# Performance work log

Measured on AMD Instinct MI355X. Metric: run time of the kernel, lower is better.

The kernel has to match this reference:

```python
import jax, jax.numpy as jnp
import numpy as np

F = 256

def setup_inputs() -> dict:
    key = jax.random.key(0)
    ks = jax.random.split(key, 6)
    s = 1.0 / np.sqrt(F)
    x = jax.random.normal(ks[0], (16, 1024, F), dtype=jnp.float32)
    W_alpha = jax.random.uniform(ks[1], (F, F), minval=-s, maxval=s, dtype=jnp.float32)
    W_beta = jax.random.uniform(ks[2], (F, F), minval=-s, maxval=s, dtype=jnp.float32)
    W_unary = jax.random.uniform(ks[3], (F, F), minval=-s, maxval=s, dtype=jnp.float32)
    b_unary = jax.random.uniform(ks[4], (F,), minval=-s, maxval=s, dtype=jnp.float32)
    W_r = jax.random.uniform(ks[5], (F, F), minval=-s, maxval=s, dtype=jnp.float32)
    return {"x": x, "W_alpha": W_alpha, "W_beta": W_beta, "W_unary": W_unary, "b_unary": b_unary, "W_r": W_r}

def reference(x, W_alpha, W_beta, W_unary, b_unary, W_r):
    # x: [B, N, F]; torch Linear computes x @ W^T (+ b)
    B, N, _ = x.shape
    alpha = jnp.einsum('bnf,gf->bng', x, W_alpha)
    beta = jnp.einsum('bnf,gf->bng', x, W_beta)
    unary = jnp.einsum('bnf,gf->bng', x, W_unary) + b_unary
    # scores: alpha_i . beta_j, diagonal excluded (i == j skipped in loop)
    scores = jnp.einsum('bif,bjf->bij', alpha, beta)
    scores = scores * (1.0 - jnp.eye(N, dtype=x.dtype))
    att = jnp.einsum('bij,bjf->bif', scores, unary) / N
    out = jnp.einsum('bif,gf->big', att, W_r) + x
    return out
```

## Files before the change

### kernel.cpp

```cpp
#include <hip/hip_runtime.h>


typedef __bf16 bf16;
typedef float floatx4 __attribute__((ext_vector_type(4)));
typedef bf16 bf16x8 __attribute__((ext_vector_type(8)));
typedef bf16 bf16x4 __attribute__((ext_vector_type(4)));

constexpr int FD = 256;
constexpr int NB = 16;
constexpr int NN = 1024;
constexpr int RR = NB * NN;

__device__ __forceinline__ bf16x8 cvt8(float4 a, float4 b) {
    bf16x8 o = { (bf16)a.x, (bf16)a.y, (bf16)a.z, (bf16)a.w,
                 (bf16)b.x, (bf16)b.y, (bf16)b.z, (bf16)b.w };
    return o;
}

__global__ __launch_bounds__(256)
void prep(const float* __restrict__ Wu, const float* __restrict__ bu, const float* __restrict__ Wr,
          bf16* __restrict__ Wcb, float* __restrict__ bc)
{
    const int blk = blockIdx.x, tid = threadIdx.x;
    if (blk < 256) {
        const int j = blk;
        float acc = 0.0f;
        for (int g = 0; g < FD; g += 4) {
            float4 wr = *(const float4*)&Wr[j * FD + g];
            acc += wr.x * Wu[g * FD + tid] + wr.y * Wu[(g + 1) * FD + tid]
                 + wr.z * Wu[(g + 2) * FD + tid] + wr.w * Wu[(g + 3) * FD + tid];
        }
        Wcb[j * FD + tid] = (bf16)acc;
    } else {
        float s = 0.0f;
        for (int g = 0; g < FD; g++) s += Wr[tid * FD + g] * bu[g];
        bc[tid] = s;
    }
}

__global__ __launch_bounds__(256)
void proj3(const float* __restrict__ x,
           const float* __restrict__ Wa, const float* __restrict__ Wb, const bf16* __restrict__ Wc,
           bf16* __restrict__ alpha, bf16* __restrict__ U2,
           bf16* __restrict__ betaT, bf16* __restrict__ U2T,
           const float* __restrict__ bc, float* __restrict__ dpart)
{
    constexpr int BM = 128, BN = 64, BK = 32, LDK = 36;
    __shared__ bf16 As[BM][LDK];
    __shared__ bf16 Bs[3][BN][LDK];
    __shared__ bf16 Tr[8960];
    const int tid = threadIdx.x;
    const int wave = tid >> 6, lane = tid & 63;
    const int q = lane >> 4, l16 = lane & 15;
    const int bm = blockIdx.y * BM, bn = blockIdx.x * BN;

    const int rowA0 = tid >> 2,          k8A0 = (tid & 3) * 8;
    const int rowA1 = (tid + 256) >> 2,  k8A1 = (tid & 3) * 8;
    const int rowW  = tid >> 2,          k8W  = (tid & 3) * 8;

    bf16x8 pxa0, pxa1, pwa, pwb; int4 pwc;
#define PROJ_LOAD(KK) do { \
        const float* s0 = &x[(size_t)(bm + rowA0) * FD + (KK) + k8A0]; \
        pxa0 = cvt8(*(const float4*)s0, *(const float4*)(s0 + 4)); \
        const float* s1 = &x[(size_t)(bm + rowA1) * FD + (KK) + k8A1]; \
        pxa1 = cvt8(*(const float4*)s1, *(const float4*)(s1 + 4)); \
        const float* sa = &Wa[(size_t)(bn + rowW) * FD + (KK) + k8W]; \
        pwa = cvt8(*(const float4*)sa, *(const float4*)(sa + 4)); \
        const float* sb = &Wb[(size_t)(bn + rowW) * FD + (KK) + k8W]; \
        pwb = cvt8(*(const float4*)sb, *(const float4*)(sb + 4)); \
        pwc = *(const int4*)&Wc[(size_t)(bn + rowW) * FD + (KK) + k8W]; \
    } while (0)

    floatx4 acc[3][2][4] = {};
    PROJ_LOAD(0);

    for (int k0 = 0; k0 < FD; k0 += BK) {
        *(bf16x8*)&As[rowA0][k8A0] = pxa0;
        *(bf16x8*)&As[rowA1][k8A1] = pxa1;
        *(bf16x8*)&Bs[0][rowW][k8W] = pwa;
        *(bf16x8*)&Bs[1][rowW][k8W] = pwb;
        *(int4*)&Bs[2][rowW][k8W] = pwc;
        __syncthreads();
        if (k0 + BK < FD) PROJ_LOAD(k0 + BK);
        bf16x8 af[2];
        #pragma unroll
        for (int mi = 0; mi < 2; mi++)
            af[mi] = *(const bf16x8*)&As[wave * 32 + mi * 16 + l16][q * 8];
        #pragma unroll
        for (int w = 0; w < 3; w++) {
            bf16x8 bq[4];
            #pragma unroll
            for (int nj = 0; nj < 4; nj++)
                bq[nj] = *(const bf16x8*)&Bs[w][nj * 16 + l16][q * 8];
            #pragma unroll
            for (int mi = 0; mi < 2; mi++)
                #pragma unroll
                for (int nj = 0; nj < 4; nj++)
                    acc[w][mi][nj] = __builtin_amdgcn_mfma_f32_16x16x32_bf16(af[mi], bq[nj], acc[w][mi][nj], 0, 0, 0);
        }
        __syncthreads();
    }
#undef PROJ_LOAD

    const int b = bm >> 10, n0 = bm & (NN - 1);
    float bcv[4];
    #pragma unroll
    for (int nj = 0; nj < 4; nj++) bcv[nj] = bc[bn + nj * 16 + l16];

    #pragma unroll
    for (int mi = 0; mi < 2; mi++)
        #pragma unroll
        for (int i = 0; i < 4; i++) {
            float p = 0.0f;
            #pragma unroll
            for (int nj = 0; nj < 4; nj++)
                p += acc[0][mi][nj][i] * acc[1][mi][nj][i];
            #pragma unroll
            for (int off = 1; off < 16; off <<= 1) p += __shfl_xor(p, off);
            if (l16 == 0) {
                int m = bm + wave * 32 + mi * 16 + q * 4 + i;
                dpart[(size_t)blockIdx.x * RR + m] = p;
            }
        }

    #pragma unroll
    for (int pass = 0; pass < 2; pass++) {
        const int w = pass ? 2 : 0;
        __syncthreads();
        #pragma unroll
        for (int mi = 0; mi < 2; mi++)
            #pragma unroll
            for (int i = 0; i < 4; i++) {
                int ml = wave * 32 + mi * 16 + q * 4 + i;
                #pragma unroll
                for (int nj = 0; nj < 4; nj++) {
                    float v = acc[w][mi][nj][i];
                    if (w == 2) v += bcv[nj];
                    Tr[ml * 68 + nj * 16 + l16] = (bf16)v;
                }
            }
        __syncthreads();
        bf16* dst = pass ? U2 : alpha;
        #pragma unroll
        for (int it = 0; it < 4; it++) {
            int c = tid + it * 256;
            int row = c >> 3, chunk = c & 7;
            bf16x8 v = *(const bf16x8*)&Tr[row * 68 + chunk * 8];
            *(bf16x8*)&dst[(size_t)(bm + row) * FD + bn + chunk * 8] = v;
        }
    }

    #pragma unroll
    for (int pass = 0; pass < 2; pass++) {
        const int w = pass ? 2 : 1;
        __syncthreads();
        #pragma unroll
        for (int mi = 0; mi < 2; mi++)
            #pragma unroll
            for (int nj = 0; nj < 4; nj++) {
                bf16x4 v4;
                #pragma unroll
                for (int i = 0; i < 4; i++) {
                    float v = acc[w][mi][nj][i];
                    if (w == 2) v += bcv[nj];
                    v4[i] = (bf16)v;
                }
                *(bf16x4*)&Tr[(nj * 16 + l16) * 140 + wave * 32 + mi * 16 + q * 4] = v4;
            }
        __syncthreads();
        bf16* dst = (pass ? U2T : betaT) + (size_t)b * FD * NN;
        #pragma unroll
        for (int it = 0; it < 4; it++) {
            int c = tid + it * 256;
            int row = c >> 4, chunk = c & 15;
            bf16x8 v = *(const bf16x8*)&Tr[row * 140 + chunk * 8];
            *(bf16x8*)&dst[(size_t)(bn + row) * NN + n0 + chunk * 8] = v;
        }
    }
}

__global__ __launch_bounds__(256)
void m2_mfma(const bf16* __restrict__ U2T, const bf16* __restrict__ betaT, bf16* __restrict__ M2t)
{
    constexpr int LDK = 36;
    __shared__ bf16 As[64][LDK];
    __shared__ bf16 Bs[64][LDK];
    __shared__ bf16 Tr[64 * 68];
    const int tid = threadIdx.x;
    const int wave = tid >> 6, lane = tid & 63;
    const int q = lane >> 4, l16 = lane & 15;
    const int wj = wave >> 1, wk = wave & 1;
    const int b = blockIdx.z;
    const int bj = blockIdx.y * 64, bk = blockIdx.x * 64;
    const int row = tid >> 2, k8 = (tid & 3) * 8;
    const bf16* Arow = U2T + (size_t)b * FD * NN + (size_t)(bj + row) * NN + k8;
    const bf16* Brow = betaT + (size_t)b * FD * NN + (size_t)(bk + row) * NN + k8;

    int4 ra = *(const int4*)&Arow[0];
    int4 rb = *(const int4*)&Brow[0];
    floatx4 acc[2][2] = {};
    for (int n0 = 0; n0 < NN; n0 += 32) {
        *(int4*)&As[row][k8] = ra;
        *(int4*)&Bs[row][k8] = rb;
        __syncthreads();
        if (n0 + 32 < NN) { ra = *(const int4*)&Arow[n0 + 32]; rb = *(const int4*)&Brow[n0 + 32]; }
        bf16x8 af[2], bq[2];
        #pragma unroll
        for (int mi = 0; mi < 2; mi++)
            af[mi] = *(const bf16x8*)&As[wj * 32 + mi * 16 + l16][q * 8];
        #pragma unroll
        for (int kj = 0; kj < 2; kj++)
            bq[kj] = *(const bf16x8*)&Bs[wk * 32 + kj * 16 + l16][q * 8];
        #pragma unroll
        for (int mi = 0; mi < 2; mi++)
            #pragma unroll
            for (int kj = 0; kj < 2; kj++)
                acc[mi][kj] = __builtin_amdgcn_mfma_f32_16x16x32_bf16(af[mi], bq[kj], acc[mi][kj], 0, 0, 0);
        __syncthreads();
    }
    __syncthreads();
    #pragma unroll
    for (int mi = 0; mi < 2; mi++)
        #pragma unroll
        for (int i = 0; i < 4; i++) {
            int jl = wj * 32 + mi * 16 + q * 4 + i;
            #pragma unroll
            for (int kj = 0; kj < 2; kj++)
                Tr[jl * 68 + wk * 32 + kj * 16 + l16] = (bf16)acc[mi][kj][i];
        }
    __syncthreads();
    bf16* Mb = M2t + (size_t)b * FD * FD;
    #pragma unroll
    for (int it = 0; it < 2; it++) {
        int c = tid + it * 256;
        int r = c >> 3, chunk = c & 7;
        bf16x8 v = *(const bf16x8*)&Tr[r * 68 + chunk * 8];
        *(bf16x8*)&Mb[(size_t)(bj + r) * FD + bk + chunk * 8] = v;
    }
}

__global__ __launch_bounds__(256)
void final_mfma(const bf16* __restrict__ alpha, const bf16* __restrict__ M2t,
                const float* __restrict__ dpart, const bf16* __restrict__ U2,
                const float* __restrict__ x, float* __restrict__ out)
{
    constexpr int BM = 128, BN = 64, BK = 32, LDK = 36;
    __shared__ bf16 As[BM][LDK];
    __shared__ bf16 Bs[BN][LDK];
    const int tid = threadIdx.x;
    const int wave = tid >> 6, lane = tid & 63;
    const int q = lane >> 4, l16 = lane & 15;
    const int bm = blockIdx.y * BM, bn = blockIdx.x * BN;
    const bf16* Qb = M2t + (size_t)(bm >> 10) * FD * FD;

    const int rowA0 = tid >> 2,         k8A0 = (tid & 3) * 8;
    const int rowA1 = (tid + 256) >> 2, k8A1 = (tid & 3) * 8;
    const int rowB  = tid >> 2,         k8B  = (tid & 3) * 8;

    int4 ra0 = *(const int4*)&alpha[(size_t)(bm + rowA0) * FD + k8A0];
    int4 ra1 = *(const int4*)&alpha[(size_t)(bm + rowA1) * FD + k8A1];
    int4 rb  = *(const int4*)&Qb[(size_t)(bn + rowB) * FD + k8B];

    floatx4 acc[2][4] = {};
    for (int k0 = 0; k0 < FD; k0 += BK) {
        *(int4*)&As[rowA0][k8A0] = ra0;
        *(int4*)&As[rowA1][k8A1] = ra1;
        *(int4*)&Bs[rowB][k8B] = rb;
        __syncthreads();
        if (k0 + BK < FD) {
            ra0 = *(const int4*)&alpha[(size_t)(bm + rowA0) * FD + k0 + BK + k8A0];
            ra1 = *(const int4*)&alpha[(size_t)(bm + rowA1) * FD + k0 + BK + k8A1];
            rb  = *(const int4*)&Qb[(size_t)(bn + rowB) * FD + k0 + BK + k8B];
        }
        bf16x8 af[2], bq[4];
        #pragma unroll
        for (int mi = 0; mi < 2; mi++)
            af[mi] = *(const bf16x8*)&As[wave * 32 + mi * 16 + l16][q * 8];
        #pragma unroll
        for (int nj = 0; nj < 4; nj++)
            bq[nj] = *(const bf16x8*)&Bs[nj * 16 + l16][q * 8];
        #pragma unroll
        for (int mi = 0; mi < 2; mi++)
            #pragma unroll
            for (int nj = 0; nj < 4; nj++)
                acc[mi][nj] = __builtin_amdgcn_mfma_f32_16x16x32_bf16(af[mi], bq[nj], acc[mi][nj], 0, 0, 0);
        __syncthreads();
    }

    #pragma unroll
    for (int mi = 0; mi < 2; mi++)
        #pragma unroll
        for (int i = 0; i < 4; i++) {
            int m = bm + wave * 32 + mi * 16 + q * 4 + i;
            float d = dpart[m] + dpart[RR + m] + dpart[2 * RR + m] + dpart[3 * RR + m];
            #pragma unroll
            for (int nj = 0; nj < 4; nj++) {
                int n = bn + nj * 16 + l16;
                float v = (acc[mi][nj][i] - d * (float)U2[(size_t)m * FD + n]) * (1.0f / 1024.0f);
                out[(size_t)m * FD + n] = v + x[(size_t)m * FD + n];
            }
        }
}

extern "C" void kernel_launch(void* const* d_in, const int* in_sizes, int n_in,
                              void* d_out, int out_size, void* d_ws, size_t ws_size,
                              hipStream_t stream)
{
    const float* x  = (const float*)d_in[0];
    const float* Wa = (const float*)d_in[1];
    const float* Wb = (const float*)d_in[2];
    const float* Wu = (const float*)d_in[3];
    const float* bu = (const float*)d_in[4];
    const float* Wr = (const float*)d_in[5];
    float* out = (float*)d_out;

    char* w = (char*)d_ws;
    bf16* Wcb   = (bf16*)w;  w += (size_t)FD * FD * 2;
    float* bc   = (float*)w; w += (size_t)FD * 4;
    bf16* alpha = (bf16*)w;  w += (size_t)RR * FD * 2;
    bf16* U2    = (bf16*)w;  w += (size_t)RR * FD * 2;
    bf16* betaT = (bf16*)w;  w += (size_t)RR * FD * 2;
    bf16* U2T   = (bf16*)w;  w += (size_t)RR * FD * 2;
    bf16* M2t   = (bf16*)w;  w += (size_t)NB * FD * FD * 2;
    float* dpart= (float*)w; w += (size_t)4 * RR * 4;

    dim3 blk(256);

    prep<<<dim3(257), blk, 0, stream>>>(Wu, bu, Wr, Wcb, bc);

    proj3<<<dim3(FD / 64, RR / 128), blk, 0, stream>>>(x, Wa, Wb, Wcb,
                                                       alpha, U2, betaT, U2T, bc, dpart);

    m2_mfma<<<dim3(FD / 64, FD / 64, NB), blk, 0, stream>>>(U2T, betaT, M2t);

    final_mfma<<<dim3(FD / 64, RR / 128), blk, 0, stream>>>(alpha, M2t, dpart, U2, x, out);
}
```

Before: 127.7 us.

## Fold W_alpha^T W_beta into one weight and drop alpha projection

Precomputes Wab = Wa^T Wb in the prep kernel, so the projection kernel computes two GEMMs (x·Wab and the unary/Wr combo) instead of three and no longer writes alpha. The final kernel reads x directly as its A operand, and the diagonal term is formed from x and the folded projection. The m2 kernel also moves to a 64-wide K tile with two MFMA sub-steps per barrier. The aim is to cut projection FLOPs and one full activation write/read, in exchange for a small extra weight-precompute kernel and a different bf16 rounding path.

Result: slower. 133.0 us (+4.1%).

```diff
diff --git a/kernel.cpp b/kernel.cpp
--- a/kernel.cpp
+++ b/kernel.cpp
@@ -18,8 +18,10 @@
 }
 
 __global__ __launch_bounds__(256)
-void prep(const float* __restrict__ Wu, const float* __restrict__ bu, const float* __restrict__ Wr,
-          bf16* __restrict__ Wcb, float* __restrict__ bc)
+void prep(const float* __restrict__ Wa, const float* __restrict__ Wb,
+          const float* __restrict__ Wu, const float* __restrict__ bu,
+          const float* __restrict__ Wr,
+          bf16* __restrict__ Wcb, bf16* __restrict__ Wab, float* __restrict__ bc)
 {
     const int blk = blockIdx.x, tid = threadIdx.x;
     if (blk < 256) {
@@ -31,23 +33,32 @@
                  + wr.z * Wu[(g + 2) * FD + tid] + wr.w * Wu[(g + 3) * FD + tid];
         }
         Wcb[j * FD + tid] = (bf16)acc;
-    } else {
+    } else if (blk == 256) {
         float s = 0.0f;
         for (int g = 0; g < FD; g++) s += Wr[tid * FD + g] * bu[g];
         bc[tid] = s;
+    } else {
+        const int f = blk - 257;
+        float acc = 0.0f;
+        for (int k = 0; k < FD; k += 4) {
+            acc += Wa[k * FD + f] * Wb[k * FD + tid]
+                 + Wa[(k + 1) * FD + f] * Wb[(k + 1) * FD + tid]
+                 + Wa[(k + 2) * FD + f] * Wb[(k + 2) * FD + tid]
+                 + Wa[(k + 3) * FD + f] * Wb[(k + 3) * FD + tid];
+        }
+        Wab[f * FD + tid] = (bf16)acc;
     }
 }
 
 __global__ __launch_bounds__(256)
-void proj3(const float* __restrict__ x,
-           const float* __restrict__ Wa, const float* __restrict__ Wb, const bf16* __restrict__ Wc,
-           bf16* __restrict__ alpha, bf16* __restrict__ U2,
-           bf16* __restrict__ betaT, bf16* __restrict__ U2T,
+void proj2(const float* __restrict__ x,
+           const bf16* __restrict__ Wab, const bf16* __restrict__ Wc,
+           bf16* __restrict__ U2, bf16* __restrict__ abT, bf16* __restrict__ U2T,
            const float* __restrict__ bc, float* __restrict__ dpart)
 {
     constexpr int BM = 128, BN = 64, BK = 32, LDK = 36;
     __shared__ bf16 As[BM][LDK];
-    __shared__ bf16 Bs[3][BN][LDK];
+    __shared__ bf16 Bs[2][BN][LDK];
     __shared__ bf16 Tr[8960];
     const int tid = threadIdx.x;
     const int wave = tid >> 6, lane = tid & 63;
@@ -58,28 +69,24 @@
     const int rowA1 = (tid + 256) >> 2,  k8A1 = (tid & 3) * 8;
     const int rowW  = tid >> 2,          k8W  = (tid & 3) * 8;
 
-    bf16x8 pxa0, pxa1, pwa, pwb; int4 pwc;
+    bf16x8 pxa0, pxa1; int4 pwq, pwc;
 #define PROJ_LOAD(KK) do { \
         const float* s0 = &x[(size_t)(bm + rowA0) * FD + (KK) + k8A0]; \
         pxa0 = cvt8(*(const float4*)s0, *(const float4*)(s0 + 4)); \
         const float* s1 = &x[(size_t)(bm + rowA1) * FD + (KK) + k8A1]; \
         pxa1 = cvt8(*(const float4*)s1, *(const float4*)(s1 + 4)); \
-        const float* sa = &Wa[(size_t)(bn + rowW) * FD + (KK) + k8W]; \
-        pwa = cvt8(*(const float4*)sa, *(const float4*)(sa + 4)); \
-        const float* sb = &Wb[(size_t)(bn + rowW) * FD + (KK) + k8W]; \
-        pwb = cvt8(*(const float4*)sb, *(const float4*)(sb + 4)); \
+        pwq = *(const int4*)&Wab[(size_t)(bn + rowW) * FD + (KK) + k8W]; \
         pwc = *(const int4*)&Wc[(size_t)(bn + rowW) * FD + (KK) + k8W]; \
     } while (0)
 
-    floatx4 acc[3][2][4] = {};
+    floatx4 acc[2][2][4] = {};
     PROJ_LOAD(0);
 
     for (int k0 = 0; k0 < FD; k0 += BK) {
         *(bf16x8*)&As[rowA0][k8A0] = pxa0;
         *(bf16x8*)&As[rowA1][k8A1] = pxa1;
-        *(bf16x8*)&Bs[0][rowW][k8W] = pwa;
-        *(bf16x8*)&Bs[1][rowW][k8W] = pwb;
-        *(int4*)&Bs[2][rowW][k8W] = pwc;
+        *(int4*)&Bs[0][rowW][k8W] = pwq;
+        *(int4*)&Bs[1][rowW][k8W] = pwc;
         __syncthreads();
         if (k0 + BK < FD) PROJ_LOAD(k0 + BK);
         bf16x8 af[2];
@@ -87,7 +94,7 @@
         for (int mi = 0; mi < 2; mi++)
             af[mi] = *(const bf16x8*)&As[wave * 32 + mi * 16 + l16][q * 8];
         #pragma unroll
-        for (int w = 0; w < 3; w++) {
+        for (int w = 0; w < 2; w++) {
             bf16x8 bq[4];
             #pragma unroll
             for (int nj = 0; nj < 4; nj++)
@@ -111,48 +118,37 @@
     for (int mi = 0; mi < 2; mi++)
         #pragma unroll
         for (int i = 0; i < 4; i++) {
+            const int m = bm + wave * 32 + mi * 16 + q * 4 + i;
             float p = 0.0f;
             #pragma unroll
             for (int nj = 0; nj < 4; nj++)
-                p += acc[0][mi][nj][i] * acc[1][mi][nj][i];
+                p += x[(size_t)m * FD + bn + nj * 16 + l16] * acc[0][mi][nj][i];
             #pragma unroll
             for (int off = 1; off < 16; off <<= 1) p += __shfl_xor(p, off);
-            if (l16 == 0) {
-                int m = bm + wave * 32 + mi * 16 + q * 4 + i;
-                dpart[(size_t)blockIdx.x * RR + m] = p;
-            }
-        }
+            if (l16 == 0) dpart[(size_t)blockIdx.x * RR + m] = p;
+        }
+
+    __syncthreads();
+    #pragma unroll
+    for (int mi = 0; mi < 2; mi++)
+        #pragma unroll
+        for (int i = 0; i < 4; i++) {
+            int ml = wave * 32 + mi * 16 + q * 4 + i;
+            #pragma unroll
+            for (int nj = 0; nj < 4; nj++)
+                Tr[ml * 68 + nj * 16 + l16] = (bf16)(acc[1][mi][nj][i] + bcv[nj]);
+        }
+    __syncthreads();
+    #pragma unroll
+    for (int it = 0; it < 4; it++) {
+        int c = tid + it * 256;
+        int row = c >> 3, chunk = c & 7;
+        bf16x8 v = *(const bf16x8*)&Tr[row * 68 + chunk * 8];
+        *(bf16x8*)&U2[(size_t)(bm + row) * FD + bn + chunk * 8] = v;
+    }
 
     #pragma unroll
     for (int pass = 0; pass < 2; pass++) {
-        const int w = pass ? 2 : 0;
-        __syncthreads();
-        #pragma unroll
-        for (int mi = 0; mi < 2; mi++)
-            #pragma unroll
-            for (int i = 0; i < 4; i++) {
-                int ml = wave * 32 + mi * 16 + q * 4 + i;
-                #pragma unroll
-                for (int nj = 0; nj < 4; nj++) {
-                    float v = acc[w][mi][nj][i];
-                    if (w == 2) v += bcv[nj];
-                    Tr[ml * 68 + nj * 16 + l16] = (bf16)v;
-                }
-            }
-        __syncthreads();
-        bf16* dst = pass ? U2 : alpha;
-        #pragma unroll
-        for (int it = 0; it < 4; it++) {
-            int c = tid + it * 256;
-            int row = c >> 3, chunk = c & 7;
-            bf16x8 v = *(const bf16x8*)&Tr[row * 68 + chunk * 8];
-            *(bf16x8*)&dst[(size_t)(bm + row) * FD + bn + chunk * 8] = v;
-        }
-    }
-
-    #pragma unroll
-    for (int pass = 0; pass < 2; pass++) {
-        const int w = pass ? 2 : 1;
         __syncthreads();
         #pragma unroll
         for (int mi = 0; mi < 2; mi++)
@@ -161,14 +157,14 @@
                 bf16x4 v4;
                 #pragma unroll
                 for (int i = 0; i < 4; i++) {
-                    float v = acc[w][mi][nj][i];
-                    if (w == 2) v += bcv[nj];
+                    float v = acc[pass][mi][nj][i];
+                    if (pass == 1) v += bcv[nj];
                     v4[i] = (bf16)v;
                 }
                 *(bf16x4*)&Tr[(nj * 16 + l16) * 140 + wave * 32 + mi * 16 + q * 4] = v4;
             }
         __syncthreads();
-        bf16* dst = (pass ? U2T : betaT) + (size_t)b * FD * NN;
+        bf16* dst = (pass ? U2T : abT) + (size_t)b * FD * NN;
         #pragma unroll
         for (int it = 0; it < 4; it++) {
             int c = tid + it * 256;
@@ -180,9 +176,9 @@
 }
 
 __global__ __launch_bounds__(256)
-void m2_mfma(const bf16* __restrict__ U2T, const bf16* __restrict__ betaT, bf16* __restrict__ M2t)
-{
-    constexpr int LDK = 36;
+void m2_mfma(const bf16* __restrict__ U2T, const bf16* __restrict__ abT, bf16* __restrict__ G)
+{
+    constexpr int LDK = 72;
     __shared__ bf16 As[64][LDK];
     __shared__ bf16 Bs[64][LDK];
     __shared__ bf16 Tr[64 * 68];
@@ -192,30 +188,45 @@
     const int wj = wave >> 1, wk = wave & 1;
     const int b = blockIdx.z;
     const int bj = blockIdx.y * 64, bk = blockIdx.x * 64;
-    const int row = tid >> 2, k8 = (tid & 3) * 8;
-    const bf16* Arow = U2T + (size_t)b * FD * NN + (size_t)(bj + row) * NN + k8;
-    const bf16* Brow = betaT + (size_t)b * FD * NN + (size_t)(bk + row) * NN + k8;
-
-    int4 ra = *(const int4*)&Arow[0];
-    int4 rb = *(const int4*)&Brow[0];
+    const int r0 = tid >> 3,         k80 = (tid & 7) * 8;
+    const int r1 = (tid + 256) >> 3, k81 = (tid & 7) * 8;
+    const bf16* Arow0 = U2T + (size_t)b * FD * NN + (size_t)(bj + r0) * NN + k80;
+    const bf16* Arow1 = U2T + (size_t)b * FD * NN + (size_t)(bj + r1) * NN + k81;
+    const bf16* Brow0 = abT + (size_t)b * FD * NN + (size_t)(bk + r0) * NN + k80;
+    const bf16* Brow1 = abT + (size_t)b * FD * NN + (size_t)(bk + r1) * NN + k81;
+
+    int4 ra0 = *(const int4*)&Arow0[0];
+    int4 ra1 = *(const int4*)&Arow1[0];
+    int4 rb0 = *(const int4*)&Brow0[0];
+    int4 rb1 = *(const int4*)&Brow1[0];
     floatx4 acc[2][2] = {};
-    for (int n0 = 0; n0 < NN; n0 += 32) {
-        *(int4*)&As[row][k8] = ra;
-        *(int4*)&Bs[row][k8] = rb;
-        __syncthreads();
-        if (n0 + 32 < NN) { ra = *(const int4*)&Arow[n0 + 32]; rb = *(const int4*)&Brow[n0 + 32]; }
-        bf16x8 af[2], bq[2];
-        #pragma unroll
-        for (int mi = 0; mi < 2; mi++)
-            af[mi] = *(const bf16x8*)&As[wj * 32 + mi * 16 + l16][q * 8];
-        #pragma unroll
-        for (int kj = 0; kj < 2; kj++)
-            bq[kj] = *(const bf16x8*)&Bs[wk * 32 + kj * 16 + l16][q * 8];
-        #pragma unroll
-        for (int mi = 0; mi < 2; mi++)
+    for (int n0 = 0; n0 < NN; n0 += 64) {
+        *(int4*)&As[r0][k80] = ra0;
+        *(int4*)&As[r1][k81] = ra1;
+        *(int4*)&Bs[r0][k80] = rb0;
+        *(int4*)&Bs[r1][k81] = rb1;
+        __syncthreads();
+        if (n0 + 64 < NN) {
+            ra0 = *(const int4*)&Arow0[n0 + 64];
+            ra1 = *(const int4*)&Arow1[n0 + 64];
+            rb0 = *(const int4*)&Brow0[n0 + 64];
+            rb1 = *(const int4*)&Brow1[n0 + 64];
+        }
+        #pragma unroll
+        for (int kk = 0; kk < 2; kk++) {
+            bf16x8 af[2], bq[2];
+            #pragma unroll
+            for (int mi = 0; mi < 2; mi++)
+                af[mi] = *(const bf16x8*)&As[wj * 32 + mi * 16 + l16][kk * 32 + q * 8];
             #pragma unroll
             for (int kj = 0; kj < 2; kj++)
-                acc[mi][kj] = __builtin_amdgcn_mfma_f32_16x16x32_bf16(af[mi], bq[kj], acc[mi][kj], 0, 0, 0);
+                bq[kj] = *(const bf16x8*)&Bs[wk * 32 + kj * 16 + l16][kk * 32 + q * 8];
+            #pragma unroll
+            for (int mi = 0; mi < 2; mi++)
+                #pragma unroll
+                for (int kj = 0; kj < 2; kj++)
+                    acc[mi][kj] = __builtin_amdgcn_mfma_f32_16x16x32_bf16(af[mi], bq[kj], acc[mi][kj], 0, 0, 0);
+        }
         __syncthreads();
     }
     __syncthreads();
@@ -229,20 +240,20 @@
                 Tr[jl * 68 + wk * 32 + kj * 16 + l16] = (bf16)acc[mi][kj][i];
         }
     __syncthreads();
-    bf16* Mb = M2t + (size_t)b * FD * FD;
+    bf16* Gb = G + (size_t)b * FD * FD;
     #pragma unroll
     for (int it = 0; it < 2; it++) {
         int c = tid + it * 256;
         int r = c >> 3, chunk = c & 7;
         bf16x8 v = *(const bf16x8*)&Tr[r * 68 + chunk * 8];
-        *(bf16x8*)&Mb[(size_t)(bj + r) * FD + bk + chunk * 8] = v;
+        *(bf16x8*)&Gb[(size_t)(bj + r) * FD + bk + chunk * 8] = v;
     }
 }
 
 __global__ __launch_bounds__(256)
-void final_mfma(const bf16* __restrict__ alpha, const bf16* __restrict__ M2t,
+void final_mfma(const float* __restrict__ x, const bf16* __restrict__ G,
                 const float* __restrict__ dpart, const bf16* __restrict__ U2,
-                const float* __restrict__ x, float* __restrict__ out)
+                float* __restrict__ out)
 {
     constexpr int BM = 128, BN = 64, BK = 32, LDK = 36;
     __shared__ bf16 As[BM][LDK];
@@ -251,27 +262,29 @@
     const int wave = tid >> 6, lane = tid & 63;
     const int q = lane >> 4, l16 = lane & 15;
     const int bm = blockIdx.y * BM, bn = blockIdx.x * BN;
-    const bf16* Qb = M2t + (size_t)(bm >> 10) * FD * FD;
+    const bf16* Gb = G + (size_t)(bm >> 10) * FD * FD;
 
     const int rowA0 = tid >> 2,         k8A0 = (tid & 3) * 8;
     const int rowA1 = (tid + 256) >> 2, k8A1 = (tid & 3) * 8;
     const int rowB  = tid >> 2,         k8B  = (tid & 3) * 8;
 
-    int4 ra0 = *(const int4*)&alpha[(size_t)(bm + rowA0) * FD + k8A0];
-    int4 ra1 = *(const int4*)&alpha[(size_t)(bm + rowA1) * FD + k8A1];
-    int4 rb  = *(const int4*)&Qb[(size_t)(bn + rowB) * FD + k8B];
+    bf16x8 ra0, ra1; int4 rb;
+#define FIN_LOAD(KK) do { \
+        const float* s0 = &x[(size_t)(bm + rowA0) * FD + (KK) + k8A0]; \
+        ra0 = cvt8(*(const float4*)s0, *(const float4*)(s0 + 4)); \
+        const float* s1 = &x[(size_t)(bm + rowA1) * FD + (KK) + k8A1]; \
+        ra1 = cvt8(*(const float4*)s1, *(const float4*)(s1 + 4)); \
+        rb = *(const int4*)&Gb[(size_t)(bn + rowB) * FD + (KK) + k8B]; \
+    } while (0)
 
     floatx4 acc[2][4] = {};
+    FIN_LOAD(0);
     for (int k0 = 0; k0 < FD; k0 += BK) {
-        *(int4*)&As[rowA0][k8A0] = ra0;
-        *(int4*)&As[rowA1][k8A1] = ra1;
+        *(bf16x8*)&As[rowA0][k8A0] = ra0;
+        *(bf16x8*)&As[rowA1][k8A1] = ra1;
         *(int4*)&Bs[rowB][k8B] = rb;
         __syncthreads();
-        if (k0 + BK < FD) {
-            ra0 = *(const int4*)&alpha[(size_t)(bm + rowA0) * FD + k0 + BK + k8A0];
-            ra1 = *(const int4*)&alpha[(size_t)(bm + rowA1) * FD + k0 + BK + k8A1];
-            rb  = *(const int4*)&Qb[(size_t)(bn + rowB) * FD + k0 + BK + k8B];
-        }
+        if (k0 + BK < FD) FIN_LOAD(k0 + BK);
         bf16x8 af[2], bq[4];
         #pragma unroll
         for (int mi = 0; mi < 2; mi++)
@@ -286,6 +299,7 @@
                 acc[mi][nj] = __builtin_amdgcn_mfma_f32_16x16x32_bf16(af[mi], bq[nj], acc[mi][nj], 0, 0, 0);
         __syncthreads();
     }
+#undef FIN_LOAD
 
     #pragma unroll
     for (int mi = 0; mi < 2; mi++)
@@ -316,22 +330,22 @@
 
     char* w = (char*)d_ws;
     bf16* Wcb   = (bf16*)w;  w += (size_t)FD * FD * 2;
+    bf16* Wab   = (bf16*)w;  w += (size_t)FD * FD * 2;
     float* bc   = (float*)w; w += (size_t)FD * 4;
-    bf16* alpha = (bf16*)w;  w += (size_t)RR * FD * 2;
     bf16* U2    = (bf16*)w;  w += (size_t)RR * FD * 2;
-    bf16* betaT = (bf16*)w;  w += (size_t)RR * FD * 2;
+    bf16* abT   = (bf16*)w;  w += (size_t)RR * FD * 2;
     bf16* U2T   = (bf16*)w;  w += (size_t)RR * FD * 2;
-    bf16* M2t   = (bf16*)w;  w += (size_t)NB * FD * FD * 2;
+    bf16* G     = (bf16*)w;  w += (size_t)NB * FD * FD * 2;
     float* dpart= (float*)w; w += (size_t)4 * RR * 4;
 
     dim3 blk(256);
 
-    prep<<<dim3(257), blk, 0, stream>>>(Wu, bu, Wr, Wcb, bc);
-
-    proj3<<<dim3(FD / 64, RR / 128), blk, 0, stream>>>(x, Wa, Wb, Wcb,
-                                                       alpha, U2, betaT, U2T, bc, dpart);
-
-    m2_mfma<<<dim3(FD / 64, FD / 64, NB), blk, 0, stream>>>(U2T, betaT, M2t);
-
-    final_mfma<<<dim3(FD / 64, RR / 128), blk, 0, stream>>>(alpha, M2t, dpart, U2, x, out);
-}
+    prep<<<dim3(513), blk, 0, stream>>>(Wa, Wb, Wu, bu, Wr, Wcb, Wab, bc);
+
+    proj2<<<dim3(FD / 64, RR / 128), blk, 0, stream>>>(x, Wab, Wcb,
+                                                       U2, abT, U2T, bc, dpart);
+
+    m2_mfma<<<dim3(FD / 64, FD / 64, NB), blk, 0, stream>>>(U2T, abT, G);
+
+    final_mfma<<<dim3(FD / 64, RR / 128), blk, 0, stream>>>(x, G, dpart, U2, out);
+}
```
